# Kernel tuning notes

Measured on AMD Instinct MI355X. Metric: run time of the kernel, lower is better.

The kernel has to match this reference:

```python
import jax, jax.numpy as jnp
import numpy as np

W_BITS = 8       # default precision = max(precisions)
MIN_PREC = 4     # min(precisions)
GROUP_SIZE = 128


def make_new_byte_indices(total_bytes: int) -> np.ndarray:
    # Replicates make_new_byte_indices_torch. Note: in the torch code,
    # argsort(argsort(new_idx)) == new_idx (it is a permutation), so the
    # "unpermute" is a gather with new_idx itself.
    bytes_per_thread = 4
    threads_per_warp = 32
    bytes_per_warp = threads_per_warp * bytes_per_thread  # 128
    full = total_bytes // bytes_per_warp * bytes_per_warp
    rem = total_bytes - full
    parts = []
    if full > 0:
        bi = np.arange(full)
        warp_offsets = (bi // bytes_per_warp) * bytes_per_warp
        thread_indices = bi % threads_per_warp
        byte_off = ((bi % bytes_per_warp) // threads_per_warp) ^ 3
        parts.append(warp_offsets + thread_indices * bytes_per_thread + byte_off)
    if rem > 0:
        ri = np.arange(rem)
        adj = rem // bytes_per_thread
        if adj > 0:
            warp_offsets = (ri // bytes_per_warp) * bytes_per_warp
            thread_indices = ri % adj
            byte_off = (ri // adj) ^ 3
            parts.append(warp_offsets + thread_indices * 4 + byte_off + full)
        else:
            parts.append(np.arange(full, full + rem))
    return np.concatenate(parts).astype(np.int64)


def dequant(qweight, scale, zero, w_bits=W_BITS):
    _, N, in_chunks = qweight.shape
    total_bytes = in_chunks * 4
    in_features = in_chunks * 32
    q = qweight[:w_bits]
    # little-endian byte view of int32 (matches torch .view(torch.uint8))
    b = jnp.stack([(q >> (8 * k)) & 0xFF for k in range(4)], axis=-1)
    b = b.reshape(w_bits, N, total_bytes)  # int32 values in [0,255]
    idx = jnp.asarray(make_new_byte_indices(total_bytes))
    b = b[:, :, idx]
    # unpack bits, MSB first within each byte
    bits = jnp.stack([(b >> i) & 1 for i in reversed(range(8))], axis=-1)
    bits = bits.reshape(w_bits, N, in_features)  # [w_bits, N, in_features]
    plane_w = jnp.asarray([1 << (w_bits - 1 - k) for k in range(w_bits)], dtype=jnp.int32)
    qw = jnp.einsum('b,bni->ni', plane_w, bits)  # int32 in [0, 2^w_bits-1]
    weight_f = qw.astype(jnp.float32)
    bit_err = w_bits - MIN_PREC
    zero = zero * (2.0 ** bit_err)
    scale_pc = jnp.repeat(scale, GROUP_SIZE, axis=1)[:, :in_features]
    zero_pc = jnp.repeat(zero, GROUP_SIZE, axis=1)[:, :in_features]
    return scale_pc * (weight_f - zero_pc)  # [N, in_features]


def setup_inputs() -> dict:
    key = jax.random.key(0)
    kx, kq, ks, kz, kb = jax.random.split(key, 5)
    B, S, IN, OUT, G = 4, 2048, 4096, 4096, GROUP_SIZE
    x = jax.random.normal(kx, (B, S, IN), dtype=jnp.float32)
    qweight = jax.random.randint(kq, (8, OUT, IN // 32), 0, 2147483647, dtype=jnp.int32)
    scale = jax.random.uniform(ks, (OUT, IN // G), dtype=jnp.float32) * 0.01 + 1e-4
    zero = jax.random.uniform(kz, (OUT, IN // G), dtype=jnp.float32) * 8.0
    bias = jax.random.normal(kb, (OUT,), dtype=jnp.float32)
    return {"x": x, "qweight": qweight, "scale": scale, "zero": zero, "bias": bias}


def reference(x, qweight, scale, zero, bias):
    weight = dequant(qweight, scale, zero, W_BITS)  # [out, in]
    return jnp.matmul(x, weight.T) + bias
```

## Files before the change

kernel.cpp:

```cpp
#include <hip/hip_runtime.h>
#include <hip/hip_bf16.h>
#include <stdint.h>

typedef __attribute__((ext_vector_type(8))) short short8;
typedef __attribute__((ext_vector_type(4))) float f32x4;

#define M_DIM 8192
#define N_DIM 4096
#define K_DIM 4096
#define BM 256
#define BN 256
#define BK 64
#define NT (K_DIM / BK)

static __device__ __forceinline__ unsigned short f32_to_bf16(float f) {
  union { float f; unsigned int u; } v; v.f = f;
  unsigned int u = v.u;
  u += 0x7fffu + ((u >> 16) & 1u);
  return (unsigned short)(u >> 16);
}

__global__ void cast_x_kernel(const float* __restrict__ x,
                              unsigned short* __restrict__ xb) {
  size_t i = ((size_t)blockIdx.x * blockDim.x + threadIdx.x) * 8;
  if (i >= (size_t)M_DIM * K_DIM) return;
  float4 v0 = *reinterpret_cast<const float4*>(x + i);
  float4 v1 = *reinterpret_cast<const float4*>(x + i + 4);
  short8 o;
  o[0] = (short)f32_to_bf16(v0.x);
  o[1] = (short)f32_to_bf16(v0.y);
  o[2] = (short)f32_to_bf16(v0.z);
  o[3] = (short)f32_to_bf16(v0.w);
  o[4] = (short)f32_to_bf16(v1.x);
  o[5] = (short)f32_to_bf16(v1.y);
  o[6] = (short)f32_to_bf16(v1.z);
  o[7] = (short)f32_to_bf16(v1.w);
  *reinterpret_cast<short8*>(xb + i) = o;
}

__global__ void dequant_kernel(const int* __restrict__ qw,
                               const float* __restrict__ scale,
                               const float* __restrict__ zero,
                               unsigned short* __restrict__ W) {
  int idx = blockIdx.x * blockDim.x + threadIdx.x;
  if (idx >= N_DIM * 128) return;
  int n = idx >> 7;
  int c = idx & 127;
  unsigned int w[8];
#pragma unroll
  for (int k = 0; k < 8; ++k)
    w[k] = (unsigned int)qw[(size_t)k * (N_DIM * 128) + idx];
  int wp = c >> 5, t = c & 31;
#pragma unroll
  for (int s = 0; s < 4; ++s) {
    int r = s ^ 3;
    unsigned int by[8];
#pragma unroll
    for (int k = 0; k < 8; ++k) by[k] = (w[k] >> (8 * r)) & 0xffu;
    int ibase = wp * 1024 + s * 256 + t * 8;
    int g = ibase >> 7;
    float sc = scale[n * 32 + g];
    float zp = zero[n * 32 + g] * 16.0f;
    short8 o;
#pragma unroll
    for (int u = 0; u < 8; ++u) {
      unsigned int q = 0;
#pragma unroll
      for (int k = 0; k < 8; ++k)
        q |= ((by[k] >> (7 - u)) & 1u) << (7 - k);
      o[u] = (short)f32_to_bf16(sc * ((float)q - zp));
    }
    *reinterpret_cast<short8*>(&W[(size_t)n * K_DIM + ibase]) = o;
  }
}


static __device__ __forceinline__ void stage_half(
    const unsigned short* __restrict__ G, int grow_base, int k0,
    char* lds_region, int tid) {
#pragma unroll
  for (int i = 0; i < 2; ++i) {
    int lr = i * 64 + (tid >> 3);
    int sslot = (tid & 7) ^ (lr & 7);
    const unsigned short* src = G + (size_t)(grow_base + lr) * K_DIM + k0 + sslot * 8;
    __builtin_amdgcn_global_load_lds(
        (const __attribute__((address_space(1))) void*)src,
        (__attribute__((address_space(3))) void*)(lds_region + i * 8192 + (tid >> 6) * 1024),
        16, 0, 0);
  }
}

#define VMCNT4 asm volatile("s_waitcnt vmcnt(4)" ::: "memory")
#define VMCNT0 asm volatile("s_waitcnt vmcnt(0)" ::: "memory")
#define NOOP ((void)0)

#define LDS_A(BUF, H) (smem + ((BUF)*2 + (H)) * 16384)
#define LDS_B(BUF, H) (smem + 65536 + ((BUF)*2 + (H)) * 16384)
#define STG_A(BUF, H, KT) stage_half(Ag, m0 + (H)*128, (KT)*64, LDS_A(BUF, H), tid)
#define STG_B(BUF, H, KT) stage_half(Bg, n0 + (H)*128, (KT)*64, LDS_B(BUF, H), tid)

#define PHASE(BUF, QM, QN, STAGE, TAIL) do {                                   \
  short8 a_[4][2], b_[2][2];                                                   \
  const char* Ab_ = LDS_A(BUF, QM);                                            \
  const char* Bb_ = LDS_B(BUF, QN);                                            \
  _Pragma("unroll") for (int mf_ = 0; mf_ < 4; ++mf_) {                        \
    int lr_ = wrbase + mf_ * 16;                                               \
    _Pragma("unroll") for (int kk_ = 0; kk_ < 2; ++kk_)                        \
      a_[mf_][kk_] = *(const short8*)(Ab_ +                                    \
          ((((lr_) << 7) | ((kk_) << 6) | hi4) ^ xorv));                       \
  }                                                                            \
  _Pragma("unroll") for (int nf_ = 0; nf_ < 2; ++nf_) {                        \
    int lc_ = wcbase + nf_ * 16;                                               \
    _Pragma("unroll") for (int kk_ = 0; kk_ < 2; ++kk_)                        \
      b_[nf_][kk_] = *(const short8*)(Bb_ +                                    \
          ((((lc_) << 7) | ((kk_) << 6) | hi4) ^ xorv));                       \
  }                                                                            \
  STAGE;                                                                       \
  __builtin_amdgcn_s_barrier();                                                \
  asm volatile("s_waitcnt lgkmcnt(0)" ::: "memory");                           \
  __builtin_amdgcn_sched_barrier(0);                                           \
  __builtin_amdgcn_s_setprio(1);                                               \
  _Pragma("unroll") for (int mf_ = 0; mf_ < 4; ++mf_)                          \
    _Pragma("unroll") for (int nf_ = 0; nf_ < 2; ++nf_)                        \
      _Pragma("unroll") for (int kk_ = 0; kk_ < 2; ++kk_)                      \
        acc[QM][QN][mf_][nf_] = __builtin_amdgcn_mfma_f32_16x16x32_bf16(       \
            a_[mf_][kk_], b_[nf_][kk_], acc[QM][QN][mf_][nf_], 0, 0, 0);       \
  __builtin_amdgcn_s_setprio(0);                                               \
  TAIL;                                                                        \
  __builtin_amdgcn_s_barrier();                                                \
} while (0)

__global__ __launch_bounds__(512, 2) void gemm_kernel(
    const unsigned short* __restrict__ Ag,
    const unsigned short* __restrict__ Bg,
    const float* __restrict__ bias,
    float* __restrict__ C) {
  __shared__ __align__(16) char smem[131072];

  int bid = blockIdx.x;
  int cpx = gridDim.x >> 3;
  int swz = (bid & 7) * cpx + (bid >> 3);
  int tm = swz >> 4;
  int tn = swz & 15;
  int m0 = tm * BM, n0 = tn * BN;

  int tid = threadIdx.x;
  int lane = tid & 63;
  int wid = tid >> 6;
  int wr = wid >> 2, wc = wid & 3;

  const int xorv = (lane & 7) << 4;
  const int hi4 = (lane >> 4) << 4;
  const int wrbase = wr * 64 + (lane & 15);
  const int wcbase = wc * 32 + (lane & 15);

  f32x4 acc[2][2][4][2];
#pragma unroll
  for (int i = 0; i < 2; ++i)
#pragma unroll
    for (int j = 0; j < 2; ++j)
#pragma unroll
      for (int mf = 0; mf < 4; ++mf)
#pragma unroll
        for (int nf = 0; nf < 2; ++nf) acc[i][j][mf][nf] = (f32x4){0.f, 0.f, 0.f, 0.f};

  STG_A(0, 0, 0); STG_A(0, 1, 0); STG_B(0, 0, 0); STG_B(0, 1, 0);
  STG_A(1, 0, 1); STG_B(1, 0, 1);
  VMCNT4;
  __builtin_amdgcn_s_barrier();

  for (int t = 0; t < 31; ++t) {
    const int kt1 = 2 * t + 1;
    PHASE(0, 0, 0, STG_A(1, 1, kt1),     NOOP);
    PHASE(0, 0, 1, STG_B(1, 1, kt1),     NOOP);
    PHASE(0, 1, 0, STG_A(0, 0, kt1 + 1), NOOP);
    PHASE(0, 1, 1, STG_B(0, 0, kt1 + 1), VMCNT4);
    PHASE(1, 0, 0, STG_A(0, 1, kt1 + 1), NOOP);
    PHASE(1, 0, 1, STG_B(0, 1, kt1 + 1), NOOP);
    PHASE(1, 1, 0, STG_A(1, 0, kt1 + 2), NOOP);
    PHASE(1, 1, 1, STG_B(1, 0, kt1 + 2), VMCNT4);
  }
  PHASE(0, 0, 0, STG_A(1, 1, 63), NOOP);
  PHASE(0, 0, 1, STG_B(1, 1, 63), NOOP);
  PHASE(0, 1, 0, NOOP,            NOOP);
  PHASE(0, 1, 1, NOOP,            VMCNT0);
  PHASE(1, 0, 0, NOOP, NOOP);
  PHASE(1, 0, 1, NOOP, NOOP);
  PHASE(1, 1, 0, NOOP, NOOP);
  PHASE(1, 1, 1, NOOP, NOOP);

#pragma unroll
  for (int qn = 0; qn < 2; ++qn)
#pragma unroll
    for (int nf = 0; nf < 2; ++nf) {
      int gcol = n0 + qn * 128 + wc * 32 + nf * 16 + (lane & 15);
      float bv = bias[gcol];
#pragma unroll
      for (int qm = 0; qm < 2; ++qm)
#pragma unroll
        for (int mf = 0; mf < 4; ++mf) {
          int grow = m0 + qm * 128 + wr * 64 + mf * 16 + ((lane >> 4) << 2);
          f32x4 v = acc[qm][qn][mf][nf];
#pragma unroll
          for (int j = 0; j < 4; ++j)
            C[(size_t)(grow + j) * N_DIM + gcol] = v[j] + bv;
        }
    }
}

extern "C" void kernel_launch(void* const* d_in, const int* in_sizes, int n_in,
                              void* d_out, int out_size, void* d_ws, size_t ws_size,
                              hipStream_t stream) {
  const float* x       = (const float*)d_in[0];
  const int*   qweight = (const int*)d_in[1];
  const float* scale   = (const float*)d_in[2];
  const float* zero    = (const float*)d_in[3];
  const float* bias    = (const float*)d_in[4];
  float* out = (float*)d_out;

  unsigned short* Xb = (unsigned short*)d_ws;
  unsigned short* Wb = Xb + (size_t)M_DIM * K_DIM;

  cast_x_kernel<<<(M_DIM * K_DIM / 8) / 256, 256, 0, stream>>>(x, Xb);
  dequant_kernel<<<(N_DIM * 128) / 256, 256, 0, stream>>>(qweight, scale, zero, Wb);
  gemm_kernel<<<(M_DIM / BM) * (N_DIM / BN), 512, 0, stream>>>(Xb, Wb, bias, out);
}
```

Baseline: 301.1 us.

## Reuse LDS fragments across phases with serpentine quadrant order and retimed staging

```diff
diff --git a/kernel.cpp b/kernel.cpp
--- a/kernel.cpp
+++ b/kernel.cpp
@@ -11,7 +11,6 @@
 #define BM 256
 #define BN 256
 #define BK 64
-#define NT (K_DIM / BK)
 
 static __device__ __forceinline__ unsigned short f32_to_bf16(float f) {
   union { float f; unsigned int u; } v; v.f = f;
@@ -90,8 +89,9 @@
   }
 }
 
-#define VMCNT4 asm volatile("s_waitcnt vmcnt(4)" ::: "memory")
+#define VMCNT2 asm volatile("s_waitcnt vmcnt(2)" ::: "memory")
 #define VMCNT0 asm volatile("s_waitcnt vmcnt(0)" ::: "memory")
+#define LGKM8  asm volatile("s_waitcnt lgkmcnt(8)" ::: "memory")
 #define NOOP ((void)0)
 
 #define LDS_A(BUF, H) (smem + ((BUF)*2 + (H)) * 16384)
@@ -99,22 +99,26 @@
 #define STG_A(BUF, H, KT) stage_half(Ag, m0 + (H)*128, (KT)*64, LDS_A(BUF, H), tid)
 #define STG_B(BUF, H, KT) stage_half(Bg, n0 + (H)*128, (KT)*64, LDS_B(BUF, H), tid)
 
-#define PHASE(BUF, QM, QN, STAGE, TAIL) do {                                   \
-  short8 a_[4][2], b_[2][2];                                                   \
+#define LOAD_A(BUF, QM) do {                                                   \
   const char* Ab_ = LDS_A(BUF, QM);                                            \
-  const char* Bb_ = LDS_B(BUF, QN);                                            \
   _Pragma("unroll") for (int mf_ = 0; mf_ < 4; ++mf_) {                        \
     int lr_ = wrbase + mf_ * 16;                                               \
     _Pragma("unroll") for (int kk_ = 0; kk_ < 2; ++kk_)                        \
       a_[mf_][kk_] = *(const short8*)(Ab_ +                                    \
           ((((lr_) << 7) | ((kk_) << 6) | hi4) ^ xorv));                       \
-  }                                                                            \
+  } } while (0)
+
+#define LOAD_B(BUF, QN) do {                                                   \
+  const char* Bb_ = LDS_B(BUF, QN);                                            \
   _Pragma("unroll") for (int nf_ = 0; nf_ < 2; ++nf_) {                        \
     int lc_ = wcbase + nf_ * 16;                                               \
     _Pragma("unroll") for (int kk_ = 0; kk_ < 2; ++kk_)                        \
       b_[nf_][kk_] = *(const short8*)(Bb_ +                                    \
           ((((lc_) << 7) | ((kk_) << 6) | hi4) ^ xorv));                       \
-  }                                                                            \
+  } } while (0)
+
+#define PHASE(LOADS, QM, QN, STAGE, TAIL) do {                                 \
+  LOADS;                                                                       \
   STAGE;                                                                       \
   __builtin_amdgcn_s_barrier();                                                \
   asm volatile("s_waitcnt lgkmcnt(0)" ::: "memory");                           \
@@ -154,6 +158,7 @@
   const int wrbase = wr * 64 + (lane & 15);
   const int wcbase = wc * 32 + (lane & 15);
 
+  short8 a_[4][2], b_[2][2];
   f32x4 acc[2][2][4][2];
 #pragma unroll
   for (int i = 0; i < 2; ++i)
@@ -165,29 +170,29 @@
         for (int nf = 0; nf < 2; ++nf) acc[i][j][mf][nf] = (f32x4){0.f, 0.f, 0.f, 0.f};
 
   STG_A(0, 0, 0); STG_A(0, 1, 0); STG_B(0, 0, 0); STG_B(0, 1, 0);
-  STG_A(1, 0, 1); STG_B(1, 0, 1);
-  VMCNT4;
+  STG_A(1, 0, 1);
+  VMCNT2;
   __builtin_amdgcn_s_barrier();
 
   for (int t = 0; t < 31; ++t) {
     const int kt1 = 2 * t + 1;
-    PHASE(0, 0, 0, STG_A(1, 1, kt1),     NOOP);
-    PHASE(0, 0, 1, STG_B(1, 1, kt1),     NOOP);
-    PHASE(0, 1, 0, STG_A(0, 0, kt1 + 1), NOOP);
-    PHASE(0, 1, 1, STG_B(0, 0, kt1 + 1), VMCNT4);
-    PHASE(1, 0, 0, STG_A(0, 1, kt1 + 1), NOOP);
-    PHASE(1, 0, 1, STG_B(0, 1, kt1 + 1), NOOP);
-    PHASE(1, 1, 0, STG_A(1, 0, kt1 + 2), NOOP);
-    PHASE(1, 1, 1, STG_B(1, 0, kt1 + 2), VMCNT4);
+    PHASE(LOAD_A(0,0); LOAD_B(0,0), 0, 0, STG_B(1,0,kt1); LGKM8, NOOP);
+    PHASE(LOAD_B(0,1),              0, 1, STG_A(1,1,kt1),        NOOP);
+    PHASE(LOAD_A(0,1),              1, 1, STG_B(1,1,kt1),        NOOP);
+    PHASE(LOAD_B(0,0),              1, 0, STG_A(0,0,kt1+1),      VMCNT2);
+    PHASE(LOAD_A(1,0); LOAD_B(1,0), 0, 0, STG_B(0,1,kt1+1); LGKM8, NOOP);
+    PHASE(LOAD_B(1,1),              0, 1, STG_A(0,1,kt1+1),      NOOP);
+    PHASE(LOAD_A(1,1),              1, 1, STG_B(0,0,kt1+1),      NOOP);
+    PHASE(LOAD_B(1,0),              1, 0, STG_A(1,0,kt1+2),      VMCNT2);
   }
-  PHASE(0, 0, 0, STG_A(1, 1, 63), NOOP);
-  PHASE(0, 0, 1, STG_B(1, 1, 63), NOOP);
-  PHASE(0, 1, 0, NOOP,            NOOP);
-  PHASE(0, 1, 1, NOOP,            VMCNT0);
-  PHASE(1, 0, 0, NOOP, NOOP);
-  PHASE(1, 0, 1, NOOP, NOOP);
-  PHASE(1, 1, 0, NOOP, NOOP);
-  PHASE(1, 1, 1, NOOP, NOOP);
+  PHASE(LOAD_A(0,0); LOAD_B(0,0), 0, 0, STG_B(1,0,63); LGKM8, NOOP);
+  PHASE(LOAD_B(0,1),              0, 1, STG_A(1,1,63),        NOOP);
+  PHASE(LOAD_A(0,1),              1, 1, STG_B(1,1,63),        NOOP);
+  PHASE(LOAD_B(0,0),              1, 0, NOOP,                 VMCNT0);
+  PHASE(LOAD_A(1,0); LOAD_B(1,0), 0, 0, NOOP, NOOP);
+  PHASE(LOAD_B(1,1),              0, 1, NOOP, NOOP);
+  PHASE(LOAD_A(1,1),              1, 1, NOOP, NOOP);
+  PHASE(LOAD_B(1,0),              1, 0, NOOP, NOOP);
 
 #pragma unroll
   for (int qn = 0; qn < 2; ++qn)
```

Result: faster. 277.4 us (-7.9%).
